# Performance work log

Measured on AMD Instinct MI355X. Metric: run time of the kernel, lower is better.

## Reference

```python
import jax, jax.numpy as jnp
import numpy as np

N = 100000      # nodes
E = 1600000     # directed edges (avg degree 16)
D_IN, D_H, D_OUT = 128, 128, 64


def glorot(k, fi, fo):
    s = (6.0 / (fi + fo)) ** 0.5
    return jax.random.uniform(k, (fi, fo), jnp.float32, -s, s)


def setup_inputs() -> dict:
    key = jax.random.key(0)
    ks = jax.random.split(key, 5)
    edges = jax.random.randint(ks[0], (2, E), 0, N)
    features = jax.random.normal(ks[1], (N, D_IN), dtype=jnp.float32)
    return dict(
        edges=edges,
        features=features,
        W0=glorot(ks[2], D_IN, D_H), b0=jnp.zeros((D_H,), jnp.float32),
        W1=glorot(ks[3], D_H, D_H), b1=jnp.zeros((D_H,), jnp.float32),
        W2=glorot(ks[4], D_H, D_OUT), b2=jnp.zeros((D_OUT,), jnp.float32),
    )


def _prep(edges):
    # add self-loops and compute symmetric GCN normalization D^-1/2 A_hat D^-1/2
    loop = jnp.arange(N)
    row = jnp.concatenate([edges[0], loop])  # source
    col = jnp.concatenate([edges[1], loop])  # target
    deg = jax.ops.segment_sum(jnp.ones((row.shape[0],), jnp.float32), col, num_segments=N)
    dinv = jnp.where(deg > 0, jax.lax.rsqrt(deg), 0.0)
    norm = dinv[row] * dinv[col]             # per-edge coefficient
    return row, col, norm


def gcn_conv(x, row, col, norm, W, b):
    x = x @ W                                 # [N, out]
    msg = x[row] * norm[:, None]              # gather + scale, [E+N, out]
    return jax.ops.segment_sum(msg, col, num_segments=N) + b


def reference(edges, features, W0, b0, W1, b1, W2, b2):
    row, col, norm = _prep(edges)
    h = jax.nn.relu(gcn_conv(features, row, col, norm, W0, b0))
    h = jax.nn.relu(gcn_conv(h, row, col, norm, W1, b1))
    h = gcn_conv(h, row, col, norm, W2, b2)
    return jax.nn.log_softmax(h, axis=1)
```

## Files before the change

### kernel.cpp

```cpp
#include <hip/hip_runtime.h>
#include <hip/hip_fp16.h>
#include <math.h>

#define NN 100000
#define EE 1600000
#define NB2 782
#define BN 128
#define NPART 512
#define CAP 2560

typedef __attribute__((ext_vector_type(8))) _Float16 half8;
typedef __attribute__((ext_vector_type(4))) float f32x4;

__device__ inline unsigned short f2h(float x) {
    return __half_as_ushort(__float2half(x));
}
__device__ inline __half2 u2h2(unsigned u) {
    return __builtin_bit_cast(__half2, u);
}
__device__ inline unsigned h22u(__half2 h) {
    return __builtin_bit_cast(unsigned, h);
}


__global__ void prep_weights(const float* __restrict__ W0, const float* __restrict__ W1,
                             const float* __restrict__ W2, unsigned short* __restrict__ Wt0,
                             unsigned short* __restrict__ Wt1, unsigned short* __restrict__ Wt2,
                             int* __restrict__ bcount) {
    int g = blockIdx.x * 256 + threadIdx.x;
    if (g < NB2) bcount[g] = 0;
    if (g < 16384) {
        int n = g >> 7, k = g & 127;
        Wt0[g] = f2h(W0[k * 128 + n]);
    } else if (g < 32768) {
        int i = g - 16384;
        int n = i >> 7, k = i & 127;
        Wt1[i] = f2h(W1[k * 128 + n]);
    } else if (g < 40960) {
        int i = g - 32768;
        int n = i >> 7, k = i & 127;
        Wt2[i] = f2h(W2[k * 64 + n]);
    }
}


__global__ __launch_bounds__(256) void scatter_bump(const int* __restrict__ src,
                                                    const int* __restrict__ dst,
                                                    int* __restrict__ bcount,
                                                    int* __restrict__ P, int e) {
    __shared__ int cnt[NB2];
    __shared__ int basep[NB2];
    __shared__ int cur[NB2];
    int t = threadIdx.x;
    for (int i = t; i < NB2; i += 256) { cnt[i] = 0; cur[i] = 0; }
    __syncthreads();
    int chunk = (e + NPART - 1) / NPART;
    int b0 = blockIdx.x * chunk, b1 = min(e, b0 + chunk);
    for (int i = b0 + t; i < b1; i += 256)
        atomicAdd(&cnt[dst[i] >> 7], 1);
    __syncthreads();
    for (int i = t; i < NB2; i += 256) {
        int c = cnt[i];
        basep[i] = c ? atomicAdd(&bcount[i], c) : 0;
    }
    __syncthreads();
    for (int i = b0 + t; i < b1; i += 256) {
        int d = dst[i];
        int b = d >> 7;
        int p = basep[b] + atomicAdd(&cur[b], 1);
        P[(size_t)b * CAP + p] = (src[i] << 7) | (d & 127);
    }
}

__global__ __launch_bounds__(256) void bucket_build(const int* __restrict__ P,
                                                    const int* __restrict__ bcount,
                                                    int2* __restrict__ offs2,
                                                    float* __restrict__ dinv,
                                                    int* __restrict__ csr, int n) {
    __shared__ int cnt[BN];
    __shared__ int sc[BN];
    __shared__ int cur[BN];
    __shared__ int stage[CAP];
    int b = blockIdx.x, t = threadIdx.x;
    int base = b * CAP;
    int count = bcount[b];
    if (t < BN) cnt[t] = 0;
    __syncthreads();
    for (int i = t; i < count; i += 256)
        atomicAdd(&cnt[P[base + i] & 127], 1);
    __syncthreads();
    int v = 0;
    if (t < BN) {
        v = cnt[t];
        sc[t] = v;
    }
    for (int d = 1; d < BN; d <<= 1) {
        __syncthreads();
        int x = (t < BN && t >= d) ? sc[t - d] : 0;
        __syncthreads();
        if (t < BN) sc[t] += x;
    }
    __syncthreads();
    if (t < BN) {
        int myoff = sc[t] - v;
        int node = b * BN + t;
        if (node < n) {
            offs2[node] = make_int2(base + myoff, base + myoff + v);
            dinv[node] = 1.0f / sqrtf((float)(v + 1));
        }
        cur[t] = myoff;
    }
    __syncthreads();
    for (int i = t; i < count; i += 256) {
        int pe = P[base + i];
        int p = atomicAdd(&cur[pe & 127], 1);
        stage[p] = ((unsigned)pe) >> 7;
    }
    __syncthreads();
    for (int i = t; i < count; i += 256) csr[base + i] = stage[i];
}

template <int DOUT, bool A_IS_F32>
__global__ __launch_bounds__(256) void gemm_mfma(const void* __restrict__ Aptr,
                                                 const unsigned short* __restrict__ Wt,
                                                 const float* __restrict__ dinv,
                                                 unsigned short* __restrict__ Y, int nrows) {
    constexpr int KP = 136;
    constexpr int NT = DOUT / 16;
    __shared__ unsigned short sA[128 * KP];
    __shared__ unsigned short sB[DOUT * KP];
    const int row0 = blockIdx.x * 128;
    const int tid = threadIdx.x;

    for (int i = tid; i < DOUT * 16; i += 256) {
        int n = i >> 4, c = (i & 15) * 8;
        uint4 v = *(const uint4*)(Wt + n * 128 + c);
        *(uint4*)(&sB[n * KP + c]) = v;
    }
    if (A_IS_F32) {
        const float* A = (const float*)Aptr;
        for (int i = tid; i < 128 * 32; i += 256) {
            int r = i >> 5, c = (i & 31) * 4;
            float4 v = make_float4(0.f, 0.f, 0.f, 0.f);
            if (row0 + r < nrows) v = *(const float4*)(A + (size_t)(row0 + r) * 128 + c);
            uint2 o;
            o.x = h22u(__floats2half2_rn(v.x, v.y));
            o.y = h22u(__floats2half2_rn(v.z, v.w));
            *(uint2*)(&sA[r * KP + c]) = o;
        }
    } else {
        const unsigned short* A = (const unsigned short*)Aptr;
        for (int i = tid; i < 128 * 16; i += 256) {
            int r = i >> 4, c = (i & 15) * 8;
            uint4 v = make_uint4(0u, 0u, 0u, 0u);
            if (row0 + r < nrows) v = *(const uint4*)(A + (size_t)(row0 + r) * 128 + c);
            *(uint4*)(&sA[r * KP + c]) = v;
        }
    }
    __syncthreads();

    const int wave = tid >> 6;
    const int lane = tid & 63;
    const int m0 = lane & 15;
    const int kq = (lane >> 4) * 8;

    f32x4 acc[2][NT];
#pragma unroll
    for (int rt = 0; rt < 2; ++rt)
#pragma unroll
        for (int t = 0; t < NT; ++t) acc[rt][t] = (f32x4){0.f, 0.f, 0.f, 0.f};

#pragma unroll
    for (int k0 = 0; k0 < 128; k0 += 32) {
        half8 a0 = *(const half8*)(&sA[(wave * 32 + m0) * KP + k0 + kq]);
        half8 a1 = *(const half8*)(&sA[(wave * 32 + 16 + m0) * KP + k0 + kq]);
#pragma unroll
        for (int t = 0; t < NT; ++t) {
            half8 b = *(const half8*)(&sB[(t * 16 + m0) * KP + k0 + kq]);
            acc[0][t] = __builtin_amdgcn_mfma_f32_16x16x32_f16(a0, b, acc[0][t], 0, 0, 0);
            acc[1][t] = __builtin_amdgcn_mfma_f32_16x16x32_f16(a1, b, acc[1][t], 0, 0, 0);
        }
    }

#pragma unroll
    for (int rt = 0; rt < 2; ++rt)
#pragma unroll
        for (int r = 0; r < 4; ++r) {
            int row = row0 + wave * 32 + rt * 16 + (lane >> 4) * 4 + r;
            if (row < nrows) {
                float dv = dinv[row];
#pragma unroll
                for (int t = 0; t < NT; ++t)
                    Y[(size_t)row * DOUT + t * 16 + (lane & 15)] = f2h(acc[rt][t][r] * dv);
            }
        }
}

__global__ __launch_bounds__(256) void agg128_f16(const unsigned short* __restrict__ Xp,
                                                  const int* __restrict__ csr,
                                                  const int2* __restrict__ offs2,
                                                  const float* __restrict__ dinv,
                                                  const float* __restrict__ bias,
                                                  unsigned short* __restrict__ Y, int n) {
    __shared__ int sIdx[4][64];
    int wv = threadIdx.x >> 6;
    int node = blockIdx.x * 4 + wv;
    if (node >= n) return;
    int lane = threadIdx.x & 63;
    int q = lane >> 4;
    int l = lane & 15;
    int2 se = offs2[node];
    int s = se.x, deg = se.y - se.x;
    if (lane < deg) sIdx[wv][lane] = csr[s + lane];
    int dcap = min(deg, 64);
    const int* idx = sIdx[wv];
    const __half2 hz = __floats2half2_rn(0.f, 0.f);
    __half2 aA0 = hz, aA1 = hz, aA2 = hz, aA3 = hz;
    __half2 aB0 = hz, aB1 = hz, aB2 = hz, aB3 = hz;
    int j = q;
    for (; j + 12 < dcap; j += 16) {
        int s0 = idx[j], s1 = idx[j + 4], s2 = idx[j + 8], s3 = idx[j + 12];
        uint4 u0 = *(const uint4*)(Xp + (size_t)s0 * 128 + l * 8);
        uint4 u1 = *(const uint4*)(Xp + (size_t)s1 * 128 + l * 8);
        uint4 u2 = *(const uint4*)(Xp + (size_t)s2 * 128 + l * 8);
        uint4 u3 = *(const uint4*)(Xp + (size_t)s3 * 128 + l * 8);
        aA0 = __hadd2(aA0, u2h2(u0.x)); aA1 = __hadd2(aA1, u2h2(u0.y));
        aA2 = __hadd2(aA2, u2h2(u0.z)); aA3 = __hadd2(aA3, u2h2(u0.w));
        aB0 = __hadd2(aB0, u2h2(u1.x)); aB1 = __hadd2(aB1, u2h2(u1.y));
        aB2 = __hadd2(aB2, u2h2(u1.z)); aB3 = __hadd2(aB3, u2h2(u1.w));
        aA0 = __hadd2(aA0, u2h2(u2.x)); aA1 = __hadd2(aA1, u2h2(u2.y));
        aA2 = __hadd2(aA2, u2h2(u2.z)); aA3 = __hadd2(aA3, u2h2(u2.w));
        aB0 = __hadd2(aB0, u2h2(u3.x)); aB1 = __hadd2(aB1, u2h2(u3.y));
        aB2 = __hadd2(aB2, u2h2(u3.z)); aB3 = __hadd2(aB3, u2h2(u3.w));
    }
    for (; j < dcap; j += 4) {
        int s0 = idx[j];
        uint4 u = *(const uint4*)(Xp + (size_t)s0 * 128 + l * 8);
        aA0 = __hadd2(aA0, u2h2(u.x)); aA1 = __hadd2(aA1, u2h2(u.y));
        aA2 = __hadd2(aA2, u2h2(u.z)); aA3 = __hadd2(aA3, u2h2(u.w));
    }
    for (int p = s + 64 + q; p < s + deg; p += 4) {
        int s0 = csr[p];
        uint4 u = *(const uint4*)(Xp + (size_t)s0 * 128 + l * 8);
        aB0 = __hadd2(aB0, u2h2(u.x)); aB1 = __hadd2(aB1, u2h2(u.y));
        aB2 = __hadd2(aB2, u2h2(u.z)); aB3 = __hadd2(aB3, u2h2(u.w));
    }
    if (q == 0) {
        uint4 u = *(const uint4*)(Xp + (size_t)node * 128 + l * 8);
        aB0 = __hadd2(aB0, u2h2(u.x)); aB1 = __hadd2(aB1, u2h2(u.y));
        aB2 = __hadd2(aB2, u2h2(u.z)); aB3 = __hadd2(aB3, u2h2(u.w));
    }
    float2 fA, fB;
    fA = __half22float2(aA0); fB = __half22float2(aB0);
    float r0 = fA.x + fB.x, r1 = fA.y + fB.y;
    fA = __half22float2(aA1); fB = __half22float2(aB1);
    float r2 = fA.x + fB.x, r3 = fA.y + fB.y;
    fA = __half22float2(aA2); fB = __half22float2(aB2);
    float r4 = fA.x + fB.x, r5 = fA.y + fB.y;
    fA = __half22float2(aA3); fB = __half22float2(aB3);
    float r6 = fA.x + fB.x, r7 = fA.y + fB.y;
    r0 += __shfl_xor(r0, 16); r0 += __shfl_xor(r0, 32);
    r1 += __shfl_xor(r1, 16); r1 += __shfl_xor(r1, 32);
    r2 += __shfl_xor(r2, 16); r2 += __shfl_xor(r2, 32);
    r3 += __shfl_xor(r3, 16); r3 += __shfl_xor(r3, 32);
    r4 += __shfl_xor(r4, 16); r4 += __shfl_xor(r4, 32);
    r5 += __shfl_xor(r5, 16); r5 += __shfl_xor(r5, 32);
    r6 += __shfl_xor(r6, 16); r6 += __shfl_xor(r6, 32);
    r7 += __shfl_xor(r7, 16); r7 += __shfl_xor(r7, 32);
    if (q == 0) {
        float di = dinv[node];
        float4 bA = *(const float4*)(bias + l * 8);
        float4 bB = *(const float4*)(bias + l * 8 + 4);
        r0 = fmaxf(fmaf(di, r0, bA.x), 0.f); r1 = fmaxf(fmaf(di, r1, bA.y), 0.f);
        r2 = fmaxf(fmaf(di, r2, bA.z), 0.f); r3 = fmaxf(fmaf(di, r3, bA.w), 0.f);
        r4 = fmaxf(fmaf(di, r4, bB.x), 0.f); r5 = fmaxf(fmaf(di, r5, bB.y), 0.f);
        r6 = fmaxf(fmaf(di, r6, bB.z), 0.f); r7 = fmaxf(fmaf(di, r7, bB.w), 0.f);
        uint4 o;
        o.x = h22u(__floats2half2_rn(r0, r1));
        o.y = h22u(__floats2half2_rn(r2, r3));
        o.z = h22u(__floats2half2_rn(r4, r5));
        o.w = h22u(__floats2half2_rn(r6, r7));
        *(uint4*)(Y + (size_t)node * 128 + l * 8) = o;
    }
}

__global__ __launch_bounds__(256) void agg_softmax64_f16(const unsigned short* __restrict__ Xp,
                                                         const int* __restrict__ csr,
                                                         const int2* __restrict__ offs2,
                                                         const float* __restrict__ dinv,
                                                         const float* __restrict__ bias,
                                                         float* __restrict__ out, int n) {
    __shared__ int sIdx[4][64];
    int wv = threadIdx.x >> 6;
    int node = blockIdx.x * 4 + wv;
    if (node >= n) return;
    int lane = threadIdx.x & 63;
    int g8 = lane >> 3;
    int l = lane & 7;
    int2 se = offs2[node];
    int s = se.x, deg = se.y - se.x;
    if (lane < deg) sIdx[wv][lane] = csr[s + lane];
    int dcap = min(deg, 64);
    const int* idx = sIdx[wv];
    const __half2 hz = __floats2half2_rn(0.f, 0.f);
    __half2 aA0 = hz, aA1 = hz, aA2 = hz, aA3 = hz;
    __half2 aB0 = hz, aB1 = hz, aB2 = hz, aB3 = hz;
    int j = g8;
    for (; j + 8 < dcap; j += 16) {
        int s0 = idx[j], s1 = idx[j + 8];
        uint4 u0 = *(const uint4*)(Xp + (size_t)s0 * 64 + l * 8);
        uint4 u1 = *(const uint4*)(Xp + (size_t)s1 * 64 + l * 8);
        aA0 = __hadd2(aA0, u2h2(u0.x)); aA1 = __hadd2(aA1, u2h2(u0.y));
        aA2 = __hadd2(aA2, u2h2(u0.z)); aA3 = __hadd2(aA3, u2h2(u0.w));
        aB0 = __hadd2(aB0, u2h2(u1.x)); aB1 = __hadd2(aB1, u2h2(u1.y));
        aB2 = __hadd2(aB2, u2h2(u1.z)); aB3 = __hadd2(aB3, u2h2(u1.w));
    }
    if (j < dcap) {
        int s0 = idx[j];
        uint4 u = *(const uint4*)(Xp + (size_t)s0 * 64 + l * 8);
        aA0 = __hadd2(aA0, u2h2(u.x)); aA1 = __hadd2(aA1, u2h2(u.y));
        aA2 = __hadd2(aA2, u2h2(u.z)); aA3 = __hadd2(aA3, u2h2(u.w));
    }
    for (int p = s + 64 + g8; p < s + deg; p += 8) {
        int s0 = csr[p];
        uint4 u = *(const uint4*)(Xp + (size_t)s0 * 64 + l * 8);
        aB0 = __hadd2(aB0, u2h2(u.x)); aB1 = __hadd2(aB1, u2h2(u.y));
        aB2 = __hadd2(aB2, u2h2(u.z)); aB3 = __hadd2(aB3, u2h2(u.w));
    }
    if (g8 == 0) {
        uint4 u = *(const uint4*)(Xp + (size_t)node * 64 + l * 8);
        aB0 = __hadd2(aB0, u2h2(u.x)); aB1 = __hadd2(aB1, u2h2(u.y));
        aB2 = __hadd2(aB2, u2h2(u.z)); aB3 = __hadd2(aB3, u2h2(u.w));
    }
    float2 fA, fB;
    fA = __half22float2(aA0); fB = __half22float2(aB0);
    float r0 = fA.x + fB.x, r1 = fA.y + fB.y;
    fA = __half22float2(aA1); fB = __half22float2(aB1);
    float r2 = fA.x + fB.x, r3 = fA.y + fB.y;
    fA = __half22float2(aA2); fB = __half22float2(aB2);
    float r4 = fA.x + fB.x, r5 = fA.y + fB.y;
    fA = __half22float2(aA3); fB = __half22float2(aB3);
    float r6 = fA.x + fB.x, r7 = fA.y + fB.y;
    r0 += __shfl_xor(r0, 8); r0 += __shfl_xor(r0, 16); r0 += __shfl_xor(r0, 32);
    r1 += __shfl_xor(r1, 8); r1 += __shfl_xor(r1, 16); r1 += __shfl_xor(r1, 32);
    r2 += __shfl_xor(r2, 8); r2 += __shfl_xor(r2, 16); r2 += __shfl_xor(r2, 32);
    r3 += __shfl_xor(r3, 8); r3 += __shfl_xor(r3, 16); r3 += __shfl_xor(r3, 32);
    r4 += __shfl_xor(r4, 8); r4 += __shfl_xor(r4, 16); r4 += __shfl_xor(r4, 32);
    r5 += __shfl_xor(r5, 8); r5 += __shfl_xor(r5, 16); r5 += __shfl_xor(r5, 32);
    r6 += __shfl_xor(r6, 8); r6 += __shfl_xor(r6, 16); r6 += __shfl_xor(r6, 32);
    r7 += __shfl_xor(r7, 8); r7 += __shfl_xor(r7, 16); r7 += __shfl_xor(r7, 32);
    if (g8 == 0) {
        float di = dinv[node];
        float4 bA = *(const float4*)(bias + l * 8);
        float4 bB = *(const float4*)(bias + l * 8 + 4);
        r0 = fmaf(di, r0, bA.x); r1 = fmaf(di, r1, bA.y);
        r2 = fmaf(di, r2, bA.z); r3 = fmaf(di, r3, bA.w);
        r4 = fmaf(di, r4, bB.x); r5 = fmaf(di, r5, bB.y);
        r6 = fmaf(di, r6, bB.z); r7 = fmaf(di, r7, bB.w);
        float m = fmaxf(fmaxf(fmaxf(r0, r1), fmaxf(r2, r3)), fmaxf(fmaxf(r4, r5), fmaxf(r6, r7)));
#pragma unroll
        for (int o = 4; o > 0; o >>= 1) m = fmaxf(m, __shfl_xor(m, o));
        float ssum = __expf(r0 - m) + __expf(r1 - m) + __expf(r2 - m) + __expf(r3 - m) +
                     __expf(r4 - m) + __expf(r5 - m) + __expf(r6 - m) + __expf(r7 - m);
#pragma unroll
        for (int o = 4; o > 0; o >>= 1) ssum += __shfl_xor(ssum, o);
        float lg = m + __logf(ssum);
        float4 o0 = make_float4(r0 - lg, r1 - lg, r2 - lg, r3 - lg);
        float4 o1 = make_float4(r4 - lg, r5 - lg, r6 - lg, r7 - lg);
        *(float4*)(out + (size_t)node * 64 + l * 8) = o0;
        *(float4*)(out + (size_t)node * 64 + l * 8 + 4) = o1;
    }
}


extern "C" void kernel_launch(void* const* d_in, const int* in_sizes, int n_in,
                              void* d_out, int out_size, void* d_ws, size_t ws_size,
                              hipStream_t stream) {
    const int* edges = (const int*)d_in[0];
    const float* feat = (const float*)d_in[1];
    const float* W0 = (const float*)d_in[2];
    const float* b0 = (const float*)d_in[3];
    const float* W1 = (const float*)d_in[4];
    const float* b1 = (const float*)d_in[5];
    const float* W2 = (const float*)d_in[6];
    const float* b2 = (const float*)d_in[7];

    const int N = NN;
    const int E = EE;

    char* ws = (char*)d_ws;
    int* bcount = (int*)ws;
    int2* offs2 = (int2*)(bcount + ((NB2 + 1) & ~1));
    float* dinv = (float*)(offs2 + N);
    int* P = (int*)(dinv + N);
    int* csr = P + (size_t)NB2 * CAP;
    unsigned short* Wt0 = (unsigned short*)(csr + (size_t)NB2 * CAP);
    unsigned short* Wt1 = Wt0 + 16384;
    unsigned short* Wt2 = Wt1 + 16384;
    size_t off = (size_t)((char*)(Wt2 + 8192) - ws);
    off = (off + 255) & ~(size_t)255;
    unsigned short* bufA = (unsigned short*)(ws + off);
    unsigned short* bufB = bufA + (size_t)N * 128;

    const int* esrc = edges;
    const int* edst = edges + E;

    prep_weights<<<160, 256, 0, stream>>>(W0, W1, W2, Wt0, Wt1, Wt2, bcount);
    scatter_bump<<<NPART, 256, 0, stream>>>(esrc, edst, bcount, P, E);
    bucket_build<<<NB2, 256, 0, stream>>>(P, bcount, offs2, dinv, csr, N);

    const int gemmBlocks = (N + 127) / 128;
    const int aggBlocks = (N + 3) / 4;

    gemm_mfma<128, true><<<gemmBlocks, 256, 0, stream>>>(feat, Wt0, dinv, bufA, N);
    agg128_f16<<<aggBlocks, 256, 0, stream>>>(bufA, csr, offs2, dinv, b0, bufB, N);
    gemm_mfma<128, false><<<gemmBlocks, 256, 0, stream>>>(bufB, Wt1, dinv, bufA, N);
    agg128_f16<<<aggBlocks, 256, 0, stream>>>(bufA, csr, offs2, dinv, b1, bufB, N);
    gemm_mfma<64, false><<<gemmBlocks, 256, 0, stream>>>(bufB, Wt2, dinv, bufA, N);
    agg_softmax64_f16<<<aggBlocks, 256, 0, stream>>>(bufA, csr, offs2, dinv, b2, (float*)d_out, N);
}
```

Before: 390.9 us.

## Store GEMM output in feature-chunked slabs for cache-local aggregation

The 128-wide GEMM output is written as 8 column-chunk slabs of 16 halves per node. A new aggregation kernel assigns each block a single chunk, so each gathered row piece is 32 bytes and a whole slab (about 3.2 MB) can stay cache-resident across the random neighbour gathers. The CSR indices are now read with nontemporal loads and the result is written with a nontemporal store. In exchange, the CSR indices are re-read eight times (once per chunk), each gather is narrower, and the GEMM stores become more scattered.

```diff
diff --git a/kernel.cpp b/kernel.cpp
--- a/kernel.cpp
+++ b/kernel.cpp
@@ -11,6 +11,7 @@
 
 typedef __attribute__((ext_vector_type(8))) _Float16 half8;
 typedef __attribute__((ext_vector_type(4))) float f32x4;
+typedef __attribute__((ext_vector_type(4))) unsigned int u32x4;
 
 __device__ inline unsigned short f2h(float x) {
     return __half_as_ushort(__float2half(x));
@@ -120,7 +121,7 @@
     for (int i = t; i < count; i += 256) csr[base + i] = stage[i];
 }
 
-template <int DOUT, bool A_IS_F32>
+template <int DOUT, bool A_IS_F32, bool CHUNK_OUT>
 __global__ __launch_bounds__(256) void gemm_mfma(const void* __restrict__ Aptr,
                                                  const unsigned short* __restrict__ Wt,
                                                  const float* __restrict__ dinv,
@@ -190,40 +191,46 @@
             if (row < nrows) {
                 float dv = dinv[row];
 #pragma unroll
-                for (int t = 0; t < NT; ++t)
-                    Y[(size_t)row * DOUT + t * 16 + (lane & 15)] = f2h(acc[rt][t][r] * dv);
+                for (int t = 0; t < NT; ++t) {
+                    unsigned short hv = f2h(acc[rt][t][r] * dv);
+                    if (CHUNK_OUT)
+                        Y[((size_t)t * NN + row) * 16 + (lane & 15)] = hv;
+                    else
+                        Y[(size_t)row * DOUT + t * 16 + (lane & 15)] = hv;
+                }
             }
         }
 }
 
-__global__ __launch_bounds__(256) void agg128_f16(const unsigned short* __restrict__ Xp,
-                                                  const int* __restrict__ csr,
-                                                  const int2* __restrict__ offs2,
-                                                  const float* __restrict__ dinv,
-                                                  const float* __restrict__ bias,
-                                                  unsigned short* __restrict__ Y, int n) {
-    __shared__ int sIdx[4][64];
-    int wv = threadIdx.x >> 6;
-    int node = blockIdx.x * 4 + wv;
+__global__ __launch_bounds__(256) void agg128_chunk(const unsigned short* __restrict__ Xc,
+                                                    const int* __restrict__ csr,
+                                                    const int2* __restrict__ offs2,
+                                                    const float* __restrict__ dinv,
+                                                    const float* __restrict__ bias,
+                                                    unsigned short* __restrict__ Y, int n) {
+    const int c = blockIdx.x & 7;
+    const int node = (blockIdx.x >> 3) * 32 + (threadIdx.x >> 3);
     if (node >= n) return;
-    int lane = threadIdx.x & 63;
-    int q = lane >> 4;
-    int l = lane & 15;
+    const int pair = (threadIdx.x >> 1) & 3;
+    const int h = threadIdx.x & 1;
+    const unsigned short* slab = Xc + (size_t)c * NN * 16;
+
     int2 se = offs2[node];
     int s = se.x, deg = se.y - se.x;
-    if (lane < deg) sIdx[wv][lane] = csr[s + lane];
-    int dcap = min(deg, 64);
-    const int* idx = sIdx[wv];
     const __half2 hz = __floats2half2_rn(0.f, 0.f);
     __half2 aA0 = hz, aA1 = hz, aA2 = hz, aA3 = hz;
     __half2 aB0 = hz, aB1 = hz, aB2 = hz, aB3 = hz;
-    int j = q;
-    for (; j + 12 < dcap; j += 16) {
-        int s0 = idx[j], s1 = idx[j + 4], s2 = idx[j + 8], s3 = idx[j + 12];
-        uint4 u0 = *(const uint4*)(Xp + (size_t)s0 * 128 + l * 8);
-        uint4 u1 = *(const uint4*)(Xp + (size_t)s1 * 128 + l * 8);
-        uint4 u2 = *(const uint4*)(Xp + (size_t)s2 * 128 + l * 8);
-        uint4 u3 = *(const uint4*)(Xp + (size_t)s3 * 128 + l * 8);
+    int d4 = deg >> 2;
+    for (int g = pair; g < d4; g += 4) {
+        const int* ip = csr + s + g * 4;
+        int s0 = __builtin_nontemporal_load(ip);
+        int s1 = __builtin_nontemporal_load(ip + 1);
+        int s2 = __builtin_nontemporal_load(ip + 2);
+        int s3 = __builtin_nontemporal_load(ip + 3);
+        uint4 u0 = *(const uint4*)(slab + (size_t)s0 * 16 + h * 8);
+        uint4 u1 = *(const uint4*)(slab + (size_t)s1 * 16 + h * 8);
+        uint4 u2 = *(const uint4*)(slab + (size_t)s2 * 16 + h * 8);
+        uint4 u3 = *(const uint4*)(slab + (size_t)s3 * 16 + h * 8);
         aA0 = __hadd2(aA0, u2h2(u0.x)); aA1 = __hadd2(aA1, u2h2(u0.y));
         aA2 = __hadd2(aA2, u2h2(u0.z)); aA3 = __hadd2(aA3, u2h2(u0.w));
         aB0 = __hadd2(aB0, u2h2(u1.x)); aB1 = __hadd2(aB1, u2h2(u1.y));
@@ -233,20 +240,14 @@
         aB0 = __hadd2(aB0, u2h2(u3.x)); aB1 = __hadd2(aB1, u2h2(u3.y));
         aB2 = __hadd2(aB2, u2h2(u3.z)); aB3 = __hadd2(aB3, u2h2(u3.w));
     }
-    for (; j < dcap; j += 4) {
-        int s0 = idx[j];
-        uint4 u = *(const uint4*)(Xp + (size_t)s0 * 128 + l * 8);
+    for (int j = d4 * 4 + pair; j < deg; j += 4) {
+        int s0 = __builtin_nontemporal_load(csr + s + j);
+        uint4 u = *(const uint4*)(slab + (size_t)s0 * 16 + h * 8);
         aA0 = __hadd2(aA0, u2h2(u.x)); aA1 = __hadd2(aA1, u2h2(u.y));
         aA2 = __hadd2(aA2, u2h2(u.z)); aA3 = __hadd2(aA3, u2h2(u.w));
     }
-    for (int p = s + 64 + q; p < s + deg; p += 4) {
-        int s0 = csr[p];
-        uint4 u = *(const uint4*)(Xp + (size_t)s0 * 128 + l * 8);
-        aB0 = __hadd2(aB0, u2h2(u.x)); aB1 = __hadd2(aB1, u2h2(u.y));
-        aB2 = __hadd2(aB2, u2h2(u.z)); aB3 = __hadd2(aB3, u2h2(u.w));
-    }
-    if (q == 0) {
-        uint4 u = *(const uint4*)(Xp + (size_t)node * 128 + l * 8);
+    if (pair == 0) {
+        uint4 u = *(const uint4*)(slab + (size_t)node * 16 + h * 8);
         aB0 = __hadd2(aB0, u2h2(u.x)); aB1 = __hadd2(aB1, u2h2(u.y));
         aB2 = __hadd2(aB2, u2h2(u.z)); aB3 = __hadd2(aB3, u2h2(u.w));
     }
@@ -259,28 +260,28 @@
     float r4 = fA.x + fB.x, r5 = fA.y + fB.y;
     fA = __half22float2(aA3); fB = __half22float2(aB3);
     float r6 = fA.x + fB.x, r7 = fA.y + fB.y;
-    r0 += __shfl_xor(r0, 16); r0 += __shfl_xor(r0, 32);
-    r1 += __shfl_xor(r1, 16); r1 += __shfl_xor(r1, 32);
-    r2 += __shfl_xor(r2, 16); r2 += __shfl_xor(r2, 32);
-    r3 += __shfl_xor(r3, 16); r3 += __shfl_xor(r3, 32);
-    r4 += __shfl_xor(r4, 16); r4 += __shfl_xor(r4, 32);
-    r5 += __shfl_xor(r5, 16); r5 += __shfl_xor(r5, 32);
-    r6 += __shfl_xor(r6, 16); r6 += __shfl_xor(r6, 32);
-    r7 += __shfl_xor(r7, 16); r7 += __shfl_xor(r7, 32);
-    if (q == 0) {
+    r0 += __shfl_xor(r0, 2); r0 += __shfl_xor(r0, 4);
+    r1 += __shfl_xor(r1, 2); r1 += __shfl_xor(r1, 4);
+    r2 += __shfl_xor(r2, 2); r2 += __shfl_xor(r2, 4);
+    r3 += __shfl_xor(r3, 2); r3 += __shfl_xor(r3, 4);
+    r4 += __shfl_xor(r4, 2); r4 += __shfl_xor(r4, 4);
+    r5 += __shfl_xor(r5, 2); r5 += __shfl_xor(r5, 4);
+    r6 += __shfl_xor(r6, 2); r6 += __shfl_xor(r6, 4);
+    r7 += __shfl_xor(r7, 2); r7 += __shfl_xor(r7, 4);
+    if (pair == 0) {
         float di = dinv[node];
-        float4 bA = *(const float4*)(bias + l * 8);
-        float4 bB = *(const float4*)(bias + l * 8 + 4);
+        float4 bA = *(const float4*)(bias + c * 16 + h * 8);
+        float4 bB = *(const float4*)(bias + c * 16 + h * 8 + 4);
         r0 = fmaxf(fmaf(di, r0, bA.x), 0.f); r1 = fmaxf(fmaf(di, r1, bA.y), 0.f);
         r2 = fmaxf(fmaf(di, r2, bA.z), 0.f); r3 = fmaxf(fmaf(di, r3, bA.w), 0.f);
         r4 = fmaxf(fmaf(di, r4, bB.x), 0.f); r5 = fmaxf(fmaf(di, r5, bB.y), 0.f);
         r6 = fmaxf(fmaf(di, r6, bB.z), 0.f); r7 = fmaxf(fmaf(di, r7, bB.w), 0.f);
-        uint4 o;
+        u32x4 o;
         o.x = h22u(__floats2half2_rn(r0, r1));
         o.y = h22u(__floats2half2_rn(r2, r3));
         o.z = h22u(__floats2half2_rn(r4, r5));
         o.w = h22u(__floats2half2_rn(r6, r7));
-        *(uint4*)(Y + (size_t)node * 128 + l * 8) = o;
+        __builtin_nontemporal_store(o, (u32x4*)(Y + (size_t)node * 128 + c * 16 + h * 8));
     }
 }
 
@@ -410,12 +411,13 @@
     bucket_build<<<NB2, 256, 0, stream>>>(P, bcount, offs2, dinv, csr, N);
 
     const int gemmBlocks = (N + 127) / 128;
+    const int aggChunkBlocks = 8 * ((N + 31) / 32);
     const int aggBlocks = (N + 3) / 4;
 
-    gemm_mfma<128, true><<<gemmBlocks, 256, 0, stream>>>(feat, Wt0, dinv, bufA, N);
-    agg128_f16<<<aggBlocks, 256, 0, stream>>>(bufA, csr, offs2, dinv, b0, bufB, N);
-    gemm_mfma<128, false><<<gemmBlocks, 256, 0, stream>>>(bufB, Wt1, dinv, bufA, N);
-    agg128_f16<<<aggBlocks, 256, 0, stream>>>(bufA, csr, offs2, dinv, b1, bufB, N);
-    gemm_mfma<64, false><<<gemmBlocks, 256, 0, stream>>>(bufB, Wt2, dinv, bufA, N);
+    gemm_mfma<128, true, true><<<gemmBlocks, 256, 0, stream>>>(feat, Wt0, dinv, bufA, N);
+    agg128_chunk<<<aggChunkBlocks, 256, 0, stream>>>(bufA, csr, offs2, dinv, b0, bufB, N);
+    gemm_mfma<128, false, true><<<gemmBlocks, 256, 0, stream>>>(bufB, Wt1, dinv, bufA, N);
+    agg128_chunk<<<aggChunkBlocks, 256, 0, stream>>>(bufA, csr, offs2, dinv, b1, bufB, N);
+    gemm_mfma<64, false, false><<<gemmBlocks, 256, 0, stream>>>(bufB, Wt2, dinv, bufA, N);
     agg_softmax64_f16<<<aggBlocks, 256, 0, stream>>>(bufA, csr, offs2, dinv, b2, (float*)d_out, N);
 }
```

New measurement: 530.8 us. 35.8% more time.

## Split layer-2 features into 32-column slabs and use nontemporal gathers in layer 1

Applied to the files above, without the earlier changes.

The layer-2 GEMM now writes its output column-chunked: four slabs of 32 halves per node. A new aggregation kernel handles one slab per block, with 16 threads per node, so that each pass gathers from a 6.4 MB slab that can stay in cache. Layer-1 aggregation switches its feature gathers to nontemporal loads through a template flag. The GEMM gets an output-mode template parameter. The trade-off is four times the index reads and block launches for layer 2, plus scattered 2-byte stores in the GEMM.

```diff
diff --git a/kernel.cpp b/kernel.cpp
--- a/kernel.cpp
+++ b/kernel.cpp
@@ -11,6 +11,7 @@
 
 typedef __attribute__((ext_vector_type(8))) _Float16 half8;
 typedef __attribute__((ext_vector_type(4))) float f32x4;
+typedef __attribute__((ext_vector_type(4))) unsigned int u32x4;
 
 __device__ inline unsigned short f2h(float x) {
     return __half_as_ushort(__float2half(x));
@@ -20,6 +21,11 @@
 }
 __device__ inline unsigned h22u(__half2 h) {
     return __builtin_bit_cast(unsigned, h);
+}
+template <bool NT>
+__device__ inline u32x4 ld16(const unsigned short* p) {
+    if (NT) return __builtin_nontemporal_load((const u32x4*)p);
+    return *(const u32x4*)p;
 }
 
 
@@ -120,7 +126,7 @@
     for (int i = t; i < count; i += 256) csr[base + i] = stage[i];
 }
 
-template <int DOUT, bool A_IS_F32>
+template <int DOUT, bool A_IS_F32, int OMODE>
 __global__ __launch_bounds__(256) void gemm_mfma(const void* __restrict__ Aptr,
                                                  const unsigned short* __restrict__ Wt,
                                                  const float* __restrict__ dinv,
@@ -190,12 +196,18 @@
             if (row < nrows) {
                 float dv = dinv[row];
 #pragma unroll
-                for (int t = 0; t < NT; ++t)
-                    Y[(size_t)row * DOUT + t * 16 + (lane & 15)] = f2h(acc[rt][t][r] * dv);
+                for (int t = 0; t < NT; ++t) {
+                    unsigned short hv = f2h(acc[rt][t][r] * dv);
+                    if (OMODE == 1)
+                        Y[(((size_t)(t >> 1) * NN + row) << 5) + ((t & 1) << 4) + (lane & 15)] = hv;
+                    else
+                        Y[(size_t)row * DOUT + t * 16 + (lane & 15)] = hv;
+                }
             }
         }
 }
 
+template <bool NTG>
 __global__ __launch_bounds__(256) void agg128_f16(const unsigned short* __restrict__ Xp,
                                                   const int* __restrict__ csr,
                                                   const int2* __restrict__ offs2,
@@ -220,10 +232,10 @@
     int j = q;
     for (; j + 12 < dcap; j += 16) {
         int s0 = idx[j], s1 = idx[j + 4], s2 = idx[j + 8], s3 = idx[j + 12];
-        uint4 u0 = *(const uint4*)(Xp + (size_t)s0 * 128 + l * 8);
-        uint4 u1 = *(const uint4*)(Xp + (size_t)s1 * 128 + l * 8);
-        uint4 u2 = *(const uint4*)(Xp + (size_t)s2 * 128 + l * 8);
-        uint4 u3 = *(const uint4*)(Xp + (size_t)s3 * 128 + l * 8);
+        u32x4 u0 = ld16<NTG>(Xp + (size_t)s0 * 128 + l * 8);
+        u32x4 u1 = ld16<NTG>(Xp + (size_t)s1 * 128 + l * 8);
+        u32x4 u2 = ld16<NTG>(Xp + (size_t)s2 * 128 + l * 8);
+        u32x4 u3 = ld16<NTG>(Xp + (size_t)s3 * 128 + l * 8);
         aA0 = __hadd2(aA0, u2h2(u0.x)); aA1 = __hadd2(aA1, u2h2(u0.y));
         aA2 = __hadd2(aA2, u2h2(u0.z)); aA3 = __hadd2(aA3, u2h2(u0.w));
         aB0 = __hadd2(aB0, u2h2(u1.x)); aB1 = __hadd2(aB1, u2h2(u1.y));
@@ -235,18 +247,18 @@
     }
     for (; j < dcap; j += 4) {
         int s0 = idx[j];
-        uint4 u = *(const uint4*)(Xp + (size_t)s0 * 128 + l * 8);
+        u32x4 u = ld16<NTG>(Xp + (size_t)s0 * 128 + l * 8);
         aA0 = __hadd2(aA0, u2h2(u.x)); aA1 = __hadd2(aA1, u2h2(u.y));
         aA2 = __hadd2(aA2, u2h2(u.z)); aA3 = __hadd2(aA3, u2h2(u.w));
     }
     for (int p = s + 64 + q; p < s + deg; p += 4) {
         int s0 = csr[p];
-        uint4 u = *(const uint4*)(Xp + (size_t)s0 * 128 + l * 8);
+        u32x4 u = ld16<NTG>(Xp + (size_t)s0 * 128 + l * 8);
         aB0 = __hadd2(aB0, u2h2(u.x)); aB1 = __hadd2(aB1, u2h2(u.y));
         aB2 = __hadd2(aB2, u2h2(u.z)); aB3 = __hadd2(aB3, u2h2(u.w));
     }
     if (q == 0) {
-        uint4 u = *(const uint4*)(Xp + (size_t)node * 128 + l * 8);
+        u32x4 u = ld16<NTG>(Xp + (size_t)node * 128 + l * 8);
         aB0 = __hadd2(aB0, u2h2(u.x)); aB1 = __hadd2(aB1, u2h2(u.y));
         aB2 = __hadd2(aB2, u2h2(u.z)); aB3 = __hadd2(aB3, u2h2(u.w));
     }
@@ -284,6 +296,89 @@
     }
 }
 
+__global__ __launch_bounds__(256) void agg128_c32(const unsigned short* __restrict__ Xc,
+                                                  const int* __restrict__ csr,
+                                                  const int2* __restrict__ offs2,
+                                                  const float* __restrict__ dinv,
+                                                  const float* __restrict__ bias,
+                                                  unsigned short* __restrict__ Y, int n) {
+    const int c = blockIdx.x & 3;
+    const int node = (blockIdx.x >> 2) * 16 + (threadIdx.x >> 4);
+    if (node >= n) return;
+    const int p = (threadIdx.x >> 2) & 3;
+    const int h = threadIdx.x & 3;
+    const unsigned short* slab = Xc + (size_t)c * NN * 32;
+
+    int2 se = offs2[node];
+    int s = se.x, deg = se.y - se.x;
+    const __half2 hz = __floats2half2_rn(0.f, 0.f);
+    __half2 aA0 = hz, aA1 = hz, aA2 = hz, aA3 = hz;
+    __half2 aB0 = hz, aB1 = hz, aB2 = hz, aB3 = hz;
+    int d4 = deg >> 2;
+    for (int g = p; g < d4; g += 4) {
+        const int* ip = csr + s + g * 4;
+        int s0 = __builtin_nontemporal_load(ip);
+        int s1 = __builtin_nontemporal_load(ip + 1);
+        int s2 = __builtin_nontemporal_load(ip + 2);
+        int s3 = __builtin_nontemporal_load(ip + 3);
+        u32x4 u0 = *(const u32x4*)(slab + (size_t)s0 * 32 + h * 8);
+        u32x4 u1 = *(const u32x4*)(slab + (size_t)s1 * 32 + h * 8);
+        u32x4 u2 = *(const u32x4*)(slab + (size_t)s2 * 32 + h * 8);
+        u32x4 u3 = *(const u32x4*)(slab + (size_t)s3 * 32 + h * 8);
+        aA0 = __hadd2(aA0, u2h2(u0.x)); aA1 = __hadd2(aA1, u2h2(u0.y));
+        aA2 = __hadd2(aA2, u2h2(u0.z)); aA3 = __hadd2(aA3, u2h2(u0.w));
+        aB0 = __hadd2(aB0, u2h2(u1.x)); aB1 = __hadd2(aB1, u2h2(u1.y));
+        aB2 = __hadd2(aB2, u2h2(u1.z)); aB3 = __hadd2(aB3, u2h2(u1.w));
+        aA0 = __hadd2(aA0, u2h2(u2.x)); aA1 = __hadd2(aA1, u2h2(u2.y));
+        aA2 = __hadd2(aA2, u2h2(u2.z)); aA3 = __hadd2(aA3, u2h2(u2.w));
+        aB0 = __hadd2(aB0, u2h2(u3.x)); aB1 = __hadd2(aB1, u2h2(u3.y));
+        aB2 = __hadd2(aB2, u2h2(u3.z)); aB3 = __hadd2(aB3, u2h2(u3.w));
+    }
+    for (int j = d4 * 4 + p; j < deg; j += 4) {
+        int s0 = __builtin_nontemporal_load(csr + s + j);
+        u32x4 u = *(const u32x4*)(slab + (size_t)s0 * 32 + h * 8);
+        aA0 = __hadd2(aA0, u2h2(u.x)); aA1 = __hadd2(aA1, u2h2(u.y));
+        aA2 = __hadd2(aA2, u2h2(u.z)); aA3 = __hadd2(aA3, u2h2(u.w));
+    }
+    if (p == 0) {
+        u32x4 u = *(const u32x4*)(slab + (size_t)node * 32 + h * 8);
+        aB0 = __hadd2(aB0, u2h2(u.x)); aB1 = __hadd2(aB1, u2h2(u.y));
+        aB2 = __hadd2(aB2, u2h2(u.z)); aB3 = __hadd2(aB3, u2h2(u.w));
+    }
+    float2 fA, fB;
+    fA = __half22float2(aA0); fB = __half22float2(aB0);
+    float r0 = fA.x + fB.x, r1 = fA.y + fB.y;
+    fA = __half22float2(aA1); fB = __half22float2(aB1);
+    float r2 = fA.x + fB.x, r3 = fA.y + fB.y;
+    fA = __half22float2(aA2); fB = __half22float2(aB2);
+    float r4 = fA.x + fB.x, r5 = fA.y + fB.y;
+    fA = __half22float2(aA3); fB = __half22float2(aB3);
+    float r6 = fA.x + fB.x, r7 = fA.y + fB.y;
+    r0 += __shfl_xor(r0, 4); r0 += __shfl_xor(r0, 8);
+    r1 += __shfl_xor(r1, 4); r1 += __shfl_xor(r1, 8);
+    r2 += __shfl_xor(r2, 4); r2 += __shfl_xor(r2, 8);
+    r3 += __shfl_xor(r3, 4); r3 += __shfl_xor(r3, 8);
+    r4 += __shfl_xor(r4, 4); r4 += __shfl_xor(r4, 8);
+    r5 += __shfl_xor(r5, 4); r5 += __shfl_xor(r5, 8);
+    r6 += __shfl_xor(r6, 4); r6 += __shfl_xor(r6, 8);
+    r7 += __shfl_xor(r7, 4); r7 += __shfl_xor(r7, 8);
+    if (p == 0) {
+        float di = dinv[node];
+        float4 bA = *(const float4*)(bias + c * 32 + h * 8);
+        float4 bB = *(const float4*)(bias + c * 32 + h * 8 + 4);
+        r0 = fmaxf(fmaf(di, r0, bA.x), 0.f); r1 = fmaxf(fmaf(di, r1, bA.y), 0.f);
+        r2 = fmaxf(fmaf(di, r2, bA.z), 0.f); r3 = fmaxf(fmaf(di, r3, bA.w), 0.f);
+        r4 = fmaxf(fmaf(di, r4, bB.x), 0.f); r5 = fmaxf(fmaf(di, r5, bB.y), 0.f);
+        r6 = fmaxf(fmaf(di, r6, bB.z), 0.f); r7 = fmaxf(fmaf(di, r7, bB.w), 0.f);
+        u32x4 o;
+        o.x = h22u(__floats2half2_rn(r0, r1));
+        o.y = h22u(__floats2half2_rn(r2, r3));
+        o.z = h22u(__floats2half2_rn(r4, r5));
+        o.w = h22u(__floats2half2_rn(r6, r7));
+        *(u32x4*)(Y + (size_t)node * 128 + c * 32 + h * 8) = o;
+    }
+}
+
 __global__ __launch_bounds__(256) void agg_softmax64_f16(const unsigned short* __restrict__ Xp,
                                                          const int* __restrict__ csr,
                                                          const int2* __restrict__ offs2,
@@ -411,11 +506,12 @@
 
     const int gemmBlocks = (N + 127) / 128;
     const int aggBlocks = (N + 3) / 4;
-
-    gemm_mfma<128, true><<<gemmBlocks, 256, 0, stream>>>(feat, Wt0, dinv, bufA, N);
-    agg128_f16<<<aggBlocks, 256, 0, stream>>>(bufA, csr, offs2, dinv, b0, bufB, N);
-    gemm_mfma<128, false><<<gemmBlocks, 256, 0, stream>>>(bufB, Wt1, dinv, bufA, N);
-    agg128_f16<<<aggBlocks, 256, 0, stream>>>(bufA, csr, offs2, dinv, b1, bufB, N);
-    gemm_mfma<64, false><<<gemmBlocks, 256, 0, stream>>>(bufB, Wt2, dinv, bufA, N);
+    const int c32Blocks = 4 * ((N + 15) / 16);
+
+    gemm_mfma<128, true, 0><<<gemmBlocks, 256, 0, stream>>>(feat, Wt0, dinv, bufA, N);
+    agg128_f16<true><<<aggBlocks, 256, 0, stream>>>(bufA, csr, offs2, dinv, b0, bufB, N);
+    gemm_mfma<128, false, 1><<<gemmBlocks, 256, 0, stream>>>(bufB, Wt1, dinv, bufA, N);
+    agg128_c32<<<c32Blocks, 256, 0, stream>>>(bufA, csr, offs2, dinv, b1, bufB, N);
+    gemm_mfma<64, false, 0><<<gemmBlocks, 256, 0, stream>>>(bufB, Wt2, dinv, bufA, N);
     agg_softmax64_f16<<<aggBlocks, 256, 0, stream>>>(bufA, csr, offs2, dinv, b2, (float*)d_out, N);
 }
```

Result: slower. 453.4 us (+16.0%).
